# Performance work log

Measured on AMD Instinct MI355X. Metric: run time of the kernel, lower is better.

The kernel has to match this reference:

```python
import jax, jax.numpy as jnp
import numpy as np

B, S, DIM = 1, 1024, 1024
H, G = 16, 4
HPG = H // G
DK = 64
DV = 64
L_CMP, D_STR = 32, 16      # compression block length l, stride d
L_SEL, N_SEL = 64, 8       # selection block length, num selected blocks
W_WIN = 512                # sliding window
TAU = 1.0
GATE_H = 32
SCALE = 1.0 / float(np.sqrt(DK))
S_CMP = (S - L_CMP) // D_STR + 1          # number of compressed blocks
N_BLK = (S + L_SEL - 1) // L_SEL          # number of selection blocks

# static Eq.9 mapping: fractional overlap of compressed block c with selection block m
_c0 = np.arange(S_CMP) * D_STR
_m0 = np.arange(N_BLK) * L_SEL
_ov = np.maximum(0, np.minimum(_c0[:, None] + L_CMP, _m0[None, :] + L_SEL)
                 - np.maximum(_c0[:, None], _m0[None, :]))
M_MAP = jnp.asarray(_ov.astype(np.float32) / float(L_CMP))   # [S_CMP, N_BLK]

_POOL_IDX = np.arange(S_CMP)[:, None] * D_STR + np.arange(L_CMP)[None, :]  # [S_CMP, L_CMP]


def _rope(x, pos):
    # llama-style rotary embedding; pos broadcasts against x's leading dims
    half = x.shape[-1] // 2
    inv = 1.0 / (10000.0 ** (jnp.arange(half, dtype=jnp.float32) / half))
    ang = pos[..., None] * inv
    cos, sin = jnp.cos(ang), jnp.sin(ang)
    x1, x2 = x[..., :half], x[..., half:]
    return jnp.concatenate([x1 * cos - x2 * sin, x1 * sin + x2 * cos], axis=-1)


def _masked_softmax(scores, mask):
    p = jax.nn.softmax(jnp.where(mask, scores, -1e30), axis=-1)
    return jnp.where(mask.any(axis=-1, keepdims=True), p, 0.0)


def _forward(x, wq, wk_sel, wv_sel, wk_win, wv_win, wk_cmp, wv_cmp, w_out,
             g1_w, g1_b, g2_w, g2_b):
    pos = jnp.arange(S, dtype=jnp.float32)
    t = jnp.arange(S)
    q = _rope((x @ wq.T).reshape(B, S, G, HPG, DK), pos[None, :, None, None])  # [B,S,G,h,Dk]

    def k_proj(w):
        k = jnp.transpose((x @ w.T).reshape(B, S, G, DK), (0, 2, 1, 3))  # [B,G,S,Dk]
        return _rope(k, pos[None, None, :])

    def v_proj(w):
        return jnp.transpose((x @ w.T).reshape(B, S, G, DV), (0, 2, 1, 3))  # [B,G,S,Dv]

    # --- compressed branch (phi = avg pooling over blocks of l with stride d) ---
    k_cmp = k_proj(wk_cmp); v_cmp = v_proj(wv_cmp)
    Kc = k_cmp[:, :, _POOL_IDX, :].mean(axis=3)  # [B,G,S_CMP,Dk]
    Vc = v_cmp[:, :, _POOL_IDX, :].mean(axis=3)  # [B,G,S_CMP,Dv]
    sc_cmp = jnp.einsum('bsghd,bgcd->bsghc', q, Kc) * SCALE
    cmp_mask = (jnp.arange(S_CMP) * D_STR + (L_CMP - 1))[None, :] <= t[:, None]  # [S,S_CMP]
    p_cmp = _masked_softmax(sc_cmp, cmp_mask[None, :, None, None, :])
    O_cmp = jnp.einsum('bsghc,bgcd->bsghd', p_cmp, Vc)

    # --- selection branch: map compressed scores to selection blocks (Eq.9),
    #     group-sum over heads, force block 0 + current block, top-k, gather ---
    p_slc = jnp.einsum('bsghc,cm->bsgm', p_cmp, M_MAP)  # sums over heads h -> [B,S,G,N_BLK]
    blk = jnp.arange(N_BLK)
    forced = (blk[None, :] == 0) | (blk[None, :] == (t // L_SEL)[:, None])  # [S,N_BLK]
    causal = (blk[None, :] * L_SEL) <= t[:, None]                            # [S,N_BLK]
    sel_logits = jnp.where(causal[None, :, None, :],
                           p_slc + 1e6 * forced[None, :, None, :], -1e9)
    _, top_idx = jax.lax.top_k(sel_logits, N_SEL)  # [B,S,G,N_SEL]
    tok = (top_idx[..., None] * L_SEL + jnp.arange(L_SEL)).reshape(B, S, G, N_SEL * L_SEL)
    tok_g = jnp.transpose(tok, (0, 2, 1, 3))  # [B,G,S,L]
    k_sel = k_proj(wk_sel); v_sel = v_proj(wv_sel)
    bi = jnp.arange(B)[:, None, None, None]
    gi = jnp.arange(G)[None, :, None, None]
    Kg = k_sel[bi, gi, tok_g]  # [B,G,S,L,Dk]
    Vg = v_sel[bi, gi, tok_g]  # [B,G,S,L,Dv]
    sc_sel = jnp.einsum('bsghd,bgsld->bsghl', q, Kg) * SCALE
    tok_mask = (tok <= t[None, :, None, None])[:, :, :, None, :]  # causal within gathered tokens
    p_sel = _masked_softmax(sc_sel, tok_mask)
    O_sel = jnp.einsum('bsghl,bgsld->bsghd', p_sel, Vg)

    # --- sliding window branch ---
    k_win = k_proj(wk_win); v_win = v_proj(wv_win)
    sc_win = jnp.einsum('bsghd,bgtd->bsght', q, k_win) * SCALE
    wmask = (t[None, :] <= t[:, None]) & (t[None, :] > t[:, None] - W_WIN)  # [S,S]
    p_win = _masked_softmax(sc_win, wmask[None, :, None, None, :])
    O_win = jnp.einsum('bsght,bgtd->bsghd', p_win, v_win)

    # --- gate MLP on group-pooled q ---
    qg = q.mean(axis=3)                              # [B,S,G,Dk]
    h1 = jax.nn.silu(qg @ g1_w.T + g1_b)
    glog = (h1 @ g2_w.T + g2_b) / max(TAU, 1e-6)
    pg = jax.nn.softmax(glog, axis=-1)               # [B,S,G,3]
    top2 = jax.lax.top_k(glog, 2)[0]
    peaked = jax.lax.stop_gradient((top2[..., 0] - top2[..., 1]) > 50.0)
    onehot = jax.nn.one_hot(jnp.argmax(glog, axis=-1), 3, dtype=pg.dtype)
    pg = jnp.where(peaked[..., None], onehot, pg)

    O = (pg[..., 0][..., None, None] * O_cmp
         + pg[..., 1][..., None, None] * O_sel
         + pg[..., 2][..., None, None] * O_win)      # [B,S,G,h,Dv]
    return O.reshape(B, S, H * DV) @ w_out.T


def setup_inputs() -> dict:
    key = jax.random.key(0)
    ks = jax.random.split(key, 11)
    n = lambda k, shp, s=0.02: jax.random.normal(k, shp, dtype=jnp.float32) * s
    return {
        'x': jax.random.normal(ks[0], (B, S, DIM), dtype=jnp.float32),
        'wq': n(ks[1], (H * DK, DIM)),
        'wk_sel': n(ks[2], (G * DK, DIM)),
        'wv_sel': n(ks[3], (G * DV, DIM)),
        'wk_win': n(ks[4], (G * DK, DIM)),
        'wv_win': n(ks[5], (G * DV, DIM)),
        'wk_cmp': n(ks[6], (G * DK, DIM)),
        'wv_cmp': n(ks[7], (G * DV, DIM)),
        'w_out': n(ks[8], (DIM, H * DV)),
        'g1_w': n(ks[9], (GATE_H, DK), 0.1),
        'g1_b': jnp.zeros((GATE_H,), jnp.float32),
        'g2_w': n(ks[10], (3, GATE_H), 0.05),  # xavier gain 0.1 -> small init
        'g2_b': jnp.zeros((3,), jnp.float32),
    }


def reference(x, wq, wk_sel, wv_sel, wk_win, wv_win, wk_cmp, wv_cmp, w_out,
              g1_w, g1_b, g2_w, g2_b):
    return _forward(x, wq, wk_sel, wv_sel, wk_win, wv_win, wk_cmp, wv_cmp, w_out,
                    g1_w, g1_b, g2_w, g2_b)
```

## Files before the change

### kernel.cpp

```cpp
#include <hip/hip_runtime.h>
#include <math.h>

#define SLEN   1024
#define NGRP   4
#define NHEAD  16
#define HPGRP  4
#define DKV    64
#define SCMP   63
#define NBLK   16
#define NSELK  8
#define WWIN   512
#define SCALEF 0.125f
#define QBLK   16
#define EXPOFF 8.0f

typedef __attribute__((ext_vector_type(4))) float f32x4;
typedef __attribute__((ext_vector_type(8))) short bf16x8;

__device__ __forceinline__ unsigned short f2bf(float f) {
  unsigned u = __float_as_uint(f);
  u += 0x7FFFu + ((u >> 16) & 1u);
  return (unsigned short)(u >> 16);
}
__device__ __forceinline__ unsigned pack2(float a, float b) {
  return (unsigned)f2bf(a) | ((unsigned)f2bf(b) << 16);
}
__device__ __forceinline__ bf16x8 pack8(float4 a, float4 b) {
  union { bf16x8 v; unsigned u[4]; } u;
  u.u[0] = pack2(a.x, a.y); u.u[1] = pack2(a.z, a.w);
  u.u[2] = pack2(b.x, b.y); u.u[3] = pack2(b.z, b.w);
  return u.v;
}

struct ConvJobs {
  const float* src[9];
  unsigned* dst[9];
  int n4[9];
  int cnt;
};

__global__ __launch_bounds__(256) void conv_f32_bf16(ConvJobs jb) {
  const int stride = gridDim.x * blockDim.x;
  for (int t = 0; t < jb.cnt; ++t) {
    const float4* s = (const float4*)jb.src[t];
    uint2* d = (uint2*)jb.dst[t];
    const int n4 = jb.n4[t];
    for (int i = blockIdx.x * blockDim.x + threadIdx.x; i < n4; i += stride) {
      const float4 v = s[i];
      uint2 o;
      o.x = pack2(v.x, v.y);
      o.y = pack2(v.z, v.w);
      d[i] = o;
    }
  }
}

__global__ __launch_bounds__(256) void conv_add_bf16(
    const float* __restrict__ a, const float* __restrict__ b, uint2* __restrict__ d)
{
  const int i = blockIdx.x * 256 + threadIdx.x;
  const float4 va = ((const float4*)a)[i];
  const float4 vb = ((const float4*)b)[i];
  uint2 o;
  o.x = pack2(va.x + vb.x, va.y + vb.y);
  o.y = pack2(va.z + vb.z, va.w + vb.w);
  d[i] = o;
}

__device__ __forceinline__ void gload_lds16(const unsigned short* g, unsigned short* l) {
  __builtin_amdgcn_global_load_lds(
      (const __attribute__((address_space(1))) void*)g,
      (__attribute__((address_space(3))) void*)l, 16, 0, 0);
}

__device__ __forceinline__ void gemm_mfma_body(
    const unsigned short* __restrict__ A, const unsigned short* __restrict__ W,
    float* __restrict__ C, int N, int K, int bm, int bn, int tid)
{
  __shared__ unsigned short As[3][2048];
  __shared__ unsigned short Bs[3][2048];
  const int lane = tid & 63;
  const int wave = tid >> 6;
  const int wr = wave >> 1, wc = wave & 1;

  const int sub = tid >> 6;
  const int kh  = (tid >> 4) & 3;
  const int row = tid & 15;
  const unsigned short* aSrc = A + (size_t)(bm + sub * 16 + row) * K + kh * 8;
  const unsigned short* bSrc = W + (size_t)(bn + sub * 16 + row) * K + kh * 8;
  const int slot = tid * 8;

  f32x4 acc[2][2];
#pragma unroll
  for (int m = 0; m < 2; ++m)
#pragma unroll
    for (int n = 0; n < 2; ++n) acc[m][n] = (f32x4){0.f, 0.f, 0.f, 0.f};

  const int NIT = K >> 5;
  gload_lds16(aSrc + 0,  &As[0][slot]);
  gload_lds16(bSrc + 0,  &Bs[0][slot]);
  gload_lds16(aSrc + 32, &As[1][slot]);
  gload_lds16(bSrc + 32, &Bs[1][slot]);

  for (int i = 0; i < NIT; ++i) {
    __builtin_amdgcn_sched_barrier(0);
    if (i + 1 < NIT) asm volatile("s_waitcnt vmcnt(2)" ::: "memory");
    else             asm volatile("s_waitcnt vmcnt(0)" ::: "memory");
    __builtin_amdgcn_s_barrier();
    __builtin_amdgcn_sched_barrier(0);
    if (i + 2 < NIT) {
      const int nb = (i + 2) % 3;
      gload_lds16(aSrc + (i + 2) * 32, &As[nb][slot]);
      gload_lds16(bSrc + (i + 2) * 32, &Bs[nb][slot]);
    }
    const int cur = i % 3;
    const bf16x8 a0 = *(const bf16x8*)(&As[cur][(wr * 2 + 0) * 512 + lane * 8]);
    const bf16x8 a1 = *(const bf16x8*)(&As[cur][(wr * 2 + 1) * 512 + lane * 8]);
    const bf16x8 b0 = *(const bf16x8*)(&Bs[cur][(wc * 2 + 0) * 512 + lane * 8]);
    const bf16x8 b1 = *(const bf16x8*)(&Bs[cur][(wc * 2 + 1) * 512 + lane * 8]);
    acc[0][0] = __builtin_amdgcn_mfma_f32_16x16x32_bf16(a0, b0, acc[0][0], 0, 0, 0);
    acc[0][1] = __builtin_amdgcn_mfma_f32_16x16x32_bf16(a0, b1, acc[0][1], 0, 0, 0);
    acc[1][0] = __builtin_amdgcn_mfma_f32_16x16x32_bf16(a1, b0, acc[1][0], 0, 0, 0);
    acc[1][1] = __builtin_amdgcn_mfma_f32_16x16x32_bf16(a1, b1, acc[1][1], 0, 0, 0);
  }

  const int cr = (lane >> 4) * 4;
  const int cc = lane & 15;
#pragma unroll
  for (int m = 0; m < 2; ++m)
#pragma unroll
    for (int n = 0; n < 2; ++n) {
      float* cp = C + (size_t)(bm + wr * 32 + m * 16 + cr) * N + (bn + wc * 32 + n * 16 + cc);
#pragma unroll
      for (int r = 0; r < 4; ++r) cp[(size_t)r * N] = acc[m][n][r];
    }
}

__global__ __launch_bounds__(256) void gemm_bf16(
    const unsigned short* __restrict__ A, const unsigned short* __restrict__ W,
    float* __restrict__ C, int N, int K)
{
  gemm_mfma_body(A, W, C, N, K, blockIdx.y * 64, blockIdx.x * 64, threadIdx.x);
}

struct W6 { const unsigned short* w[6]; };

__global__ __launch_bounds__(256) void gemm_bf16_kv6(
    const unsigned short* __restrict__ A, W6 p6, float* __restrict__ Cbase)
{
  gemm_mfma_body(A, p6.w[blockIdx.z], Cbase + (size_t)blockIdx.z * (SLEN * 256),
                 256, 1024, blockIdx.y * 64, blockIdx.x * 64, threadIdx.x);
}

__global__ __launch_bounds__(256) void prep_kernel(
    const float* __restrict__ qf,
    const float* __restrict__ kself,
    const float* __restrict__ kwinf,
    const float* __restrict__ g1w, const float* __restrict__ g1b,
    const float* __restrict__ g2w, const float* __restrict__ g2b,
    unsigned short* __restrict__ q_b,
    unsigned short* __restrict__ kselb, unsigned short* __restrict__ kwinb,
    float* __restrict__ gates, float2* __restrict__ tab)
{
  const int s = blockIdx.x, t = threadIdx.x;
  __shared__ float csS[32], snS[32];
  __shared__ float qs[1024];
  __shared__ float qgS[4][64];
  __shared__ float h1S[4][32];
  __shared__ float glS[4][3];
  if (t < 32) {
    const float inv = powf(10000.f, -(float)t * (1.f / 32.f));
    float sn, cs;
    sincosf((float)s * inv, &sn, &cs);
    csS[t] = cs; snS[t] = sn;
    tab[s * 32 + t] = make_float2(cs, sn);
  }
  __syncthreads();
  {
    const int ht = t >> 4;
    const float* qr = qf + (size_t)s * 1024 + ht * 64;
#pragma unroll
    for (int i = 0; i < 2; ++i) {
      const int dd = (t & 15) * 2 + i;
      const float x1 = qr[dd], x2 = qr[dd + 32];
      qs[ht * 64 + dd]      = x1 * csS[dd] - x2 * snS[dd];
      qs[ht * 64 + dd + 32] = x1 * snS[dd] + x2 * csS[dd];
    }
  }
  {
    const int which = t >> 7;
    const int g = (t >> 5) & 3, dd = t & 31;
    const float* src = (which ? kwinf : kself) + (size_t)s * 256 + g * 64;
    unsigned short* dst = (which ? kwinb : kselb) + (size_t)s * 256 + g * 64;
    const float x1 = src[dd], x2 = src[dd + 32];
    dst[dd]      = f2bf(x1 * csS[dd] - x2 * snS[dd]);
    dst[dd + 32] = f2bf(x1 * snS[dd] + x2 * csS[dd]);
  }
  __syncthreads();
  {
    uint2 o;
    o.x = pack2(qs[t * 4 + 0], qs[t * 4 + 1]);
    o.y = pack2(qs[t * 4 + 2], qs[t * 4 + 3]);
    *(uint2*)(q_b + (size_t)s * 1024 + t * 4) = o;
  }
  {
    const int g = t >> 6, d = t & 63;
    qgS[g][d] = (qs[g * 256 + d] + qs[g * 256 + 64 + d] +
                 qs[g * 256 + 128 + d] + qs[g * 256 + 192 + d]) * 0.25f;
  }
  __syncthreads();
  if (t < 128) {
    const int g = t >> 5, j = t & 31;
    float a = g1b[j];
    for (int d = 0; d < 64; ++d) a += qgS[g][d] * g1w[j * 64 + d];
    h1S[g][j] = a / (1.f + expf(-a));
  }
  __syncthreads();
  if (t < 16) {
    const int g = t >> 2, rr = t & 3;
    if (rr < 3) {
      float a = g2b[rr];
      for (int j = 0; j < 32; ++j) a += h1S[g][j] * g2w[rr * 32 + j];
      glS[g][rr] = a;
    }
  }
  __syncthreads();
  if (t < 4) {
    const int g = t;
    const float gl0 = glS[g][0], gl1 = glS[g][1], gl2 = glS[g][2];
    const float m1 = fmaxf(gl0, fmaxf(gl1, gl2));
    const float e0 = expf(gl0 - m1), e1 = expf(gl1 - m1), e2 = expf(gl2 - m1);
    const float inv = 1.f / (e0 + e1 + e2);
    float p0 = e0 * inv, p1 = e1 * inv, p2 = e2 * inv;
    int am = 0; float best = gl0;
    if (gl1 > best) { best = gl1; am = 1; }
    if (gl2 > best) { best = gl2; am = 2; }
    float second = -INFINITY;
    if (am != 0) second = fmaxf(second, gl0);
    if (am != 1) second = fmaxf(second, gl1);
    if (am != 2) second = fmaxf(second, gl2);
    if (best - second > 50.f) {
      p0 = (am == 0) ? 1.f : 0.f; p1 = (am == 1) ? 1.f : 0.f; p2 = (am == 2) ? 1.f : 0.f;
    }
    float* o = gates + (size_t)(s * 4 + g) * 3;
    o[0] = p0; o[1] = p1; o[2] = p2;
  }
}

__global__ __launch_bounds__(64) void pool_kernel(
    const float* __restrict__ kcmp, const float* __restrict__ vcmp,
    const float2* __restrict__ tab,
    unsigned short* __restrict__ KcB, unsigned short* __restrict__ VcTB)
{
  const int c = blockIdx.x;
  const int g = blockIdx.y;
  const int d = threadIdx.x;
  float ak = 0.f, av = 0.f;
  if (c < SCMP) {
    const int d2 = d & 31;
    for (int j = 0; j < 32; ++j) {
      const int pos = c * 16 + j;
      const float2 t2 = tab[pos * 32 + d2];
      const float k1 = kcmp[(size_t)pos * 256 + g * 64 + d2];
      const float k2 = kcmp[(size_t)pos * 256 + g * 64 + d2 + 32];
      ak += (d < 32) ? (k1 * t2.x - k2 * t2.y) : (k1 * t2.y + k2 * t2.x);
      av += vcmp[(size_t)pos * 256 + g * 64 + d];
    }
    ak *= (1.f / 32.f); av *= (1.f / 32.f);
  }
  KcB[(size_t)(g * 64 + c) * 64 + d] = f2bf(ak);
  VcTB[(size_t)(g * 64 + d) * 64 + c] = f2bf(av);
}

__global__ __launch_bounds__(256) void transpose_v(
    const float* __restrict__ v0, const float* __restrict__ v1,
    unsigned short* __restrict__ t0, unsigned short* __restrict__ t1)
{
  const float* src = blockIdx.z ? v1 : v0;
  unsigned short* dst = blockIdx.z ? t1 : t0;
  __shared__ float tile[32][33];
  const int tr = blockIdx.x * 32, tc = blockIdx.y * 32;
  const int r = threadIdx.x >> 5, c = threadIdx.x & 31;
#pragma unroll
  for (int i = 0; i < 4; ++i)
    tile[r + i * 8][c] = src[(size_t)(tr + r + i * 8) * 256 + tc + c];
  __syncthreads();
#pragma unroll
  for (int i = 0; i < 4; ++i)
    dst[(size_t)(tc + r + i * 8) * 1024 + tr + c] = f2bf(tile[c][r + i * 8]);
}

__device__ __forceinline__ void stage_tile(
    const unsigned short* kbase, int krow,
    const unsigned short* vbase, int vrow,
    unsigned short* Kb, unsigned short* Vb, int tid)
{
#pragma unroll
  for (int i = 0; i < 2; ++i) {
    const int t2 = tid + i * 256;
    const int sf = t2 >> 7, sks = (t2 >> 6) & 1, skh = (t2 >> 4) & 3, stk = t2 & 15;
    gload_lds16(kbase + (size_t)(16 * sf + stk) * krow + sks * 32 + skh * 8, Kb + t2 * 8);
    gload_lds16(vbase + (size_t)(16 * sf + stk) * vrow + sks * 32 + skh * 8, Vb + t2 * 8);
  }
}

template<int BR>
__device__ __forceinline__ void attn_compute(
    int b, int s0, int l,
    bf16x8 aq0, bf16x8 aq1,
    float (&ps)[4], f32x4 (&Oa)[4],
    const unsigned short* Klds, const unsigned short* Vlds,
    float (*Pw)[68], const unsigned* selmaskS)
{
  const int kg = l >> 4, lr = l & 15;
  f32x4 sc[4];
  __builtin_amdgcn_s_setprio(1);
#pragma unroll
  for (int f = 0; f < 4; ++f) {
    sc[f] = (f32x4){0.f, 0.f, 0.f, 0.f};
    sc[f] = __builtin_amdgcn_mfma_f32_16x16x32_bf16(
        aq0, *(const bf16x8*)(Klds + (f * 2 + 0) * 512 + l * 8), sc[f], 0, 0, 0);
    sc[f] = __builtin_amdgcn_mfma_f32_16x16x32_bf16(
        aq1, *(const bf16x8*)(Klds + (f * 2 + 1) * 512 + l * 8), sc[f], 0, 0, 0);
  }
  __builtin_amdgcn_s_setprio(0);

#pragma unroll
  for (int r = 0; r < 4; ++r) {
    const int lrow = kg * 4 + r;
    const int sr = s0 + lrow;
#pragma unroll
    for (int f = 0; f < 4; ++f) {
      const int tok = b * 64 + 16 * f + lr;
      bool ok;
      if (BR == 0)      ok = (tok < SCMP) && (tok * 16 + 31 <= sr);
      else if (BR == 1) ok = ((selmaskS[lrow] >> b) & 1u) && (tok <= sr);
      else              ok = (tok <= sr) && (tok > sr - WWIN);
      const float p = ok ? __expf(sc[f][r] * SCALEF - EXPOFF) : 0.f;
      Pw[lrow][16 * f + lr] = p;
      ps[r] += p;
    }
  }
  asm volatile("s_waitcnt lgkmcnt(0)" ::: "memory");
#pragma unroll
  for (int ks = 0; ks < 2; ++ks) {
    const float4 pa0 = *(const float4*)&Pw[lr][ks * 32 + kg * 8];
    const float4 pa1 = *(const float4*)&Pw[lr][ks * 32 + kg * 8 + 4];
    const bf16x8 pa = pack8(pa0, pa1);
    __builtin_amdgcn_s_setprio(1);
#pragma unroll
    for (int f = 0; f < 4; ++f)
      Oa[f] = __builtin_amdgcn_mfma_f32_16x16x32_bf16(
          pa, *(const bf16x8*)(Vlds + (f * 2 + ks) * 512 + l * 8), Oa[f], 0, 0, 0);
    __builtin_amdgcn_s_setprio(0);
  }
}

__global__ __launch_bounds__(256) void attn_mfma_kernel(
    const unsigned short* __restrict__ qb,
    const unsigned short* __restrict__ kselb,
    const unsigned short* __restrict__ vselT,
    const unsigned short* __restrict__ kwinb,
    const unsigned short* __restrict__ vwinT,
    const unsigned short* __restrict__ KcB,
    const unsigned short* __restrict__ VcTB,
    const float* __restrict__ gates,
    float* __restrict__ Ocs, float* __restrict__ Owin)
{
  const int qt = blockIdx.x;
  const int g  = blockIdx.y;
  const int z  = blockIdx.z;
  const int s0 = qt * QBLK;
  const int tid = threadIdx.x;
  const int w = tid >> 6, l = tid & 63;
  const int kg = l >> 4, lr = l & 15;
  const int bmax = s0 >> 6;

  __shared__ unsigned short Klds[2][4096];
  __shared__ unsigned short Vlds[2][4096];
  __shared__ float Plds[4][16][68];
  __shared__ float lgS[QBLK][16];
  __shared__ float lcS[4][16];
  __shared__ unsigned selmaskS[QBLK];
  __shared__ int selListS[16];
  __shared__ int nselS;

  if (tid < QBLK) selmaskS[tid] = 0u;

  const int sq = s0 + lr;
  const unsigned short* qrow = qb + (size_t)(sq * 16 + g * 4 + w) * 64;
  const bf16x8 aq0 = *(const bf16x8*)(qrow + kg * 8);
  const bf16x8 aq1 = *(const bf16x8*)(qrow + 32 + kg * 8);

  float gv[3][4];
#pragma unroll
  for (int r = 0; r < 4; ++r) {
    const int sr = s0 + kg * 4 + r;
    const float* gp = gates + (size_t)(sr * 4 + g) * 3;
    gv[0][r] = gp[0]; gv[1][r] = gp[1]; gv[2][r] = gp[2];
  }

  f32x4 Ot[4];
#pragma unroll
  for (int f = 0; f < 4; ++f) Ot[f] = (f32x4){0.f, 0.f, 0.f, 0.f};

  float ps[4], ls[4];
  f32x4 Oa[4];

#define ARESET() do { \
    _Pragma("unroll") for (int r = 0; r < 4; ++r) ps[r] = 0.f; \
    _Pragma("unroll") for (int f = 0; f < 4; ++f) Oa[f] = (f32x4){0.f,0.f,0.f,0.f}; \
  } while (0)
#define REDUCE_LS() do { \
    _Pragma("unroll") for (int r = 0; r < 4; ++r) { \
      ls[r] = ps[r]; \
      ls[r] += __shfl_xor(ls[r], 1); ls[r] += __shfl_xor(ls[r], 2); \
      ls[r] += __shfl_xor(ls[r], 4); ls[r] += __shfl_xor(ls[r], 8); } \
  } while (0)
#define AFINAL(bi) do { \
    _Pragma("unroll") for (int f = 0; f < 4; ++f) \
    _Pragma("unroll") for (int r = 0; r < 4; ++r) \
      Ot[f][r] += gv[bi][r] * ((ls[r] > 0.f) ? (Oa[f][r] / ls[r]) : 0.f); \
  } while (0)

  if (z == 0) {
    ARESET();
    stage_tile(KcB + (size_t)g * 64 * 64, 64, VcTB + (size_t)g * 64 * 64, 64,
               Klds[0], Vlds[0], tid);
    __syncthreads();
    attn_compute<0>(0, s0, l, aq0, aq1, ps, Oa, Klds[0], Vlds[0], Plds[w], selmaskS);
    REDUCE_LS();
    if ((l & 15) == 0) {
#pragma unroll
      for (int r = 0; r < 4; ++r) lcS[w][kg * 4 + r] = ls[r];
    }
    AFINAL(0);
    __syncthreads();

    {
      const int row = tid >> 4, mm = tid & 15;
      float psl = 0.f;
#pragma unroll
      for (int hh = 0; hh < 4; ++hh) {
        const float lc = lcS[hh][row];
        if (lc > 0.f) {
          const int cb = 4 * mm;
          float a = Plds[hh][row][cb] + Plds[hh][row][cb + 1] + Plds[hh][row][cb + 2];
          if (cb >= 1)       a += 0.5f * Plds[hh][row][cb - 1];
          if (cb + 3 < SCMP) a += 0.5f * Plds[hh][row][cb + 3];
          psl += a / lc;
        }
      }
      const bool causal = (mm <= bmax);
      const bool forced = (mm == 0) || (mm == bmax);
      lgS[row][mm] = causal ? (psl + (forced ? 1e6f : 0.f)) : -1e9f;
    }
    __syncthreads();
    {
      const int row = tid >> 4, mm = tid & 15;
      const float my = lgS[row][mm];
      int rank = 0;
#pragma unroll
      for (int m2 = 0; m2 < 16; ++m2) {
        const float v = lgS[row][m2];
        if (v > my || (v == my && m2 < mm)) ++rank;
      }
      if (rank < NSELK && mm <= bmax) atomicOr(&selmaskS[row], 1u << mm);
    }
    __syncthreads();
    if (tid == 0) {
      unsigned u = 0;
      for (int r = 0; r < QBLK; ++r) u |= selmaskS[r];
      int n = 0;
      for (int b = 0; b < 16; ++b) if ((u >> b) & 1u) selListS[n++] = b;
      nselS = n;
    }
    __syncthreads();
    const int nt = nselS;

    ARESET();
    {
      const int b0 = selListS[0];
      stage_tile(kselb + (size_t)b0 * 64 * 256 + g * 64, 256,
                 vselT + (size_t)g * 64 * 1024 + b0 * 64, 1024,
                 Klds[0], Vlds[0], tid);
      __syncthreads();
      for (int i = 0; i < nt; ++i) {
        if (i + 1 < nt) {
          const int bn = selListS[i + 1];
          stage_tile(kselb + (size_t)bn * 64 * 256 + g * 64, 256,
                     vselT + (size_t)g * 64 * 1024 + bn * 64, 1024,
                     Klds[(i + 1) & 1], Vlds[(i + 1) & 1], tid);
        }
        attn_compute<1>(selListS[i], s0, l, aq0, aq1, ps, Oa,
                        Klds[i & 1], Vlds[i & 1], Plds[w], selmaskS);
        __syncthreads();
      }
    }
    REDUCE_LS();
    AFINAL(1);

#pragma unroll
    for (int f = 0; f < 4; ++f)
#pragma unroll
      for (int r = 0; r < 4; ++r) {
        const int sr = s0 + kg * 4 + r;
        Ocs[(size_t)(sr * 16 + g * 4 + w) * 64 + 16 * f + lr] = Ot[f][r];
      }
  } else {
    ARESET();
    const int blo = (s0 >= (WWIN - 1)) ? ((s0 - (WWIN - 1)) >> 6) : 0;
    const int nt = bmax - blo + 1;
    stage_tile(kwinb + (size_t)blo * 64 * 256 + g * 64, 256,
               vwinT + (size_t)g * 64 * 1024 + blo * 64, 1024,
               Klds[0], Vlds[0], tid);
    __syncthreads();
    for (int i = 0; i < nt; ++i) {
      if (i + 1 < nt) {
        const int bn = blo + i + 1;
        stage_tile(kwinb + (size_t)bn * 64 * 256 + g * 64, 256,
                   vwinT + (size_t)g * 64 * 1024 + bn * 64, 1024,
                   Klds[(i + 1) & 1], Vlds[(i + 1) & 1], tid);
      }
      attn_compute<2>(blo + i, s0, l, aq0, aq1, ps, Oa,
                      Klds[i & 1], Vlds[i & 1], Plds[w], selmaskS);
      __syncthreads();
    }
    REDUCE_LS();
    AFINAL(2);

#pragma unroll
    for (int f = 0; f < 4; ++f)
#pragma unroll
      for (int r = 0; r < 4; ++r) {
        const int sr = s0 + kg * 4 + r;
        Owin[(size_t)(sr * 16 + g * 4 + w) * 64 + 16 * f + lr] = Ot[f][r];
      }
  }
#undef ARESET
#undef REDUCE_LS
#undef AFINAL
}

extern "C" void kernel_launch(void* const* d_in, const int* in_sizes, int n_in,
                              void* d_out, int out_size, void* d_ws, size_t ws_size,
                              hipStream_t stream) {
  const float* x      = (const float*)d_in[0];
  const float* wq     = (const float*)d_in[1];
  const float* wk_sel = (const float*)d_in[2];
  const float* wv_sel = (const float*)d_in[3];
  const float* wk_win = (const float*)d_in[4];
  const float* wv_win = (const float*)d_in[5];
  const float* wk_cmp = (const float*)d_in[6];
  const float* wv_cmp = (const float*)d_in[7];
  const float* w_out  = (const float*)d_in[8];
  const float* g1w    = (const float*)d_in[9];
  const float* g1b    = (const float*)d_in[10];
  const float* g2w    = (const float*)d_in[11];
  const float* g2b    = (const float*)d_in[12];

  float* ws = (float*)d_ws;
  float* q     = ws;
  float* kv    = q + 1048576;
  float* ksel  = kv;
  float* vsel  = kv + 1 * 262144;
  float* kwin  = kv + 2 * 262144;
  float* vwin  = kv + 3 * 262144;
  float* kcmp  = kv + 4 * 262144;
  float* vcmp  = kv + 5 * 262144;
  float* gts   = kv + 6 * 262144;
  float* Obuf  = gts + 12288;
  float* Owin  = kv;
  float2* tab  = (float2*)Obuf;

  unsigned short* xb     = (unsigned short*)(Obuf + 1048576);
  unsigned short* wqb    = xb + 1048576;
  unsigned short* kvwb   = wqb + 1048576;
  unsigned short* w_outb = kvwb + 6 * 262144;
  unsigned short* q_b    = w_outb + 1048576;
  unsigned short* kselb  = q_b + 1048576;
  unsigned short* kwinb  = kselb + 262144;
  unsigned short* vselT  = kwinb + 262144;
  unsigned short* vwinT  = vselT + 262144;
  unsigned short* KcB    = vwinT + 262144;
  unsigned short* VcTB   = KcB + 16384;

  ConvJobs j1 = {};
  j1.cnt = 9;
  j1.src[0] = x;      j1.dst[0] = (unsigned*)xb;                j1.n4[0] = 262144;
  j1.src[1] = wq;     j1.dst[1] = (unsigned*)wqb;               j1.n4[1] = 262144;
  j1.src[2] = wk_sel; j1.dst[2] = (unsigned*)(kvwb + 0*262144); j1.n4[2] = 65536;
  j1.src[3] = wv_sel; j1.dst[3] = (unsigned*)(kvwb + 1*262144); j1.n4[3] = 65536;
  j1.src[4] = wk_win; j1.dst[4] = (unsigned*)(kvwb + 2*262144); j1.n4[4] = 65536;
  j1.src[5] = wv_win; j1.dst[5] = (unsigned*)(kvwb + 3*262144); j1.n4[5] = 65536;
  j1.src[6] = wk_cmp; j1.dst[6] = (unsigned*)(kvwb + 4*262144); j1.n4[6] = 65536;
  j1.src[7] = wv_cmp; j1.dst[7] = (unsigned*)(kvwb + 5*262144); j1.n4[7] = 65536;
  j1.src[8] = w_out;  j1.dst[8] = (unsigned*)w_outb;            j1.n4[8] = 262144;
  conv_f32_bf16<<<1024, 256, 0, stream>>>(j1);

  gemm_bf16<<<dim3(16, 16), 256, 0, stream>>>(xb, wqb, q, 1024, 1024);
  W6 p6 = {{ kvwb + 0*262144, kvwb + 1*262144, kvwb + 2*262144,
             kvwb + 3*262144, kvwb + 4*262144, kvwb + 5*262144 }};
  gemm_bf16_kv6<<<dim3(4, 16, 6), 256, 0, stream>>>(xb, p6, kv);

  prep_kernel<<<1024, 256, 0, stream>>>(q, ksel, kwin, g1w, g1b, g2w, g2b,
                                        q_b, kselb, kwinb, gts, tab);

  pool_kernel<<<dim3(64, 4), 64, 0, stream>>>(kcmp, vcmp, tab, KcB, VcTB);

  transpose_v<<<dim3(32, 8, 2), 256, 0, stream>>>(vsel, vwin, vselT, vwinT);

  attn_mfma_kernel<<<dim3(64, 4, 2), 256, 0, stream>>>(
      q_b, kselb, vselT, kwinb, vwinT, KcB, VcTB, gts, Obuf, Owin);

  conv_add_bf16<<<1024, 256, 0, stream>>>(Obuf, Owin, (uint2*)xb);
  gemm_bf16<<<dim3(16, 16), 256, 0, stream>>>(xb, w_outb, (float*)d_out, 1024, 1024);
}
```

Measured before the change: 122.4 us.

## Fuse Q/KV projections into one GEMM, merge prep kernels, triple-buffer attention tiles

```diff
diff --git a/kernel.cpp b/kernel.cpp
--- a/kernel.cpp
+++ b/kernel.cpp
@@ -13,6 +13,7 @@
 #define SCALEF 0.125f
 #define QBLK   16
 #define EXPOFF 8.0f
+#define CSTR   2560
 
 typedef __attribute__((ext_vector_type(4))) float f32x4;
 typedef __attribute__((ext_vector_type(8))) short bf16x8;
@@ -143,151 +144,148 @@
   gemm_mfma_body(A, W, C, N, K, blockIdx.y * 64, blockIdx.x * 64, threadIdx.x);
 }
 
-struct W6 { const unsigned short* w[6]; };
-
-__global__ __launch_bounds__(256) void gemm_bf16_kv6(
-    const unsigned short* __restrict__ A, W6 p6, float* __restrict__ Cbase)
-{
-  gemm_mfma_body(A, p6.w[blockIdx.z], Cbase + (size_t)blockIdx.z * (SLEN * 256),
-                 256, 1024, blockIdx.y * 64, blockIdx.x * 64, threadIdx.x);
-}
-
-__global__ __launch_bounds__(256) void prep_kernel(
-    const float* __restrict__ qf,
-    const float* __restrict__ kself,
-    const float* __restrict__ kwinf,
+__global__ __launch_bounds__(256) void mid_kernel(
+    const float* __restrict__ C,
     const float* __restrict__ g1w, const float* __restrict__ g1b,
     const float* __restrict__ g2w, const float* __restrict__ g2b,
     unsigned short* __restrict__ q_b,
     unsigned short* __restrict__ kselb, unsigned short* __restrict__ kwinb,
-    float* __restrict__ gates, float2* __restrict__ tab)
+    float* __restrict__ gates,
+    unsigned short* __restrict__ vselT, unsigned short* __restrict__ vwinT,
+    unsigned short* __restrict__ KcB, unsigned short* __restrict__ VcTB)
 {
-  const int s = blockIdx.x, t = threadIdx.x;
+  const int b = blockIdx.x;
+  const int t = threadIdx.x;
+
   __shared__ float csS[32], snS[32];
   __shared__ float qs[1024];
   __shared__ float qgS[4][64];
   __shared__ float h1S[4][32];
   __shared__ float glS[4][3];
-  if (t < 32) {
-    const float inv = powf(10000.f, -(float)t * (1.f / 32.f));
-    float sn, cs;
-    sincosf((float)s * inv, &sn, &cs);
-    csS[t] = cs; snS[t] = sn;
-    tab[s * 32 + t] = make_float2(cs, sn);
-  }
-  __syncthreads();
-  {
-    const int ht = t >> 4;
-    const float* qr = qf + (size_t)s * 1024 + ht * 64;
-#pragma unroll
-    for (int i = 0; i < 2; ++i) {
-      const int dd = (t & 15) * 2 + i;
-      const float x1 = qr[dd], x2 = qr[dd + 32];
-      qs[ht * 64 + dd]      = x1 * csS[dd] - x2 * snS[dd];
-      qs[ht * 64 + dd + 32] = x1 * snS[dd] + x2 * csS[dd];
-    }
-  }
-  {
-    const int which = t >> 7;
-    const int g = (t >> 5) & 3, dd = t & 31;
-    const float* src = (which ? kwinf : kself) + (size_t)s * 256 + g * 64;
-    unsigned short* dst = (which ? kwinb : kselb) + (size_t)s * 256 + g * 64;
-    const float x1 = src[dd], x2 = src[dd + 32];
-    dst[dd]      = f2bf(x1 * csS[dd] - x2 * snS[dd]);
-    dst[dd + 32] = f2bf(x1 * snS[dd] + x2 * csS[dd]);
-  }
-  __syncthreads();
-  {
-    uint2 o;
-    o.x = pack2(qs[t * 4 + 0], qs[t * 4 + 1]);
-    o.y = pack2(qs[t * 4 + 2], qs[t * 4 + 3]);
-    *(uint2*)(q_b + (size_t)s * 1024 + t * 4) = o;
-  }
-  {
+  __shared__ float tile[32][33];
+  __shared__ float csP[32][32], snP[32][32];
+
+  if (b < 1024) {
+    const int s = b;
+    if (t < 32) {
+      const float inv = powf(10000.f, -(float)t * (1.f / 32.f));
+      float sn, cs;
+      sincosf((float)s * inv, &sn, &cs);
+      csS[t] = cs; snS[t] = sn;
+    }
+    __syncthreads();
+    {
+      const int ht = t >> 4;
+      const float* qr = C + (size_t)s * CSTR + ht * 64;
+#pragma unroll
+      for (int i = 0; i < 2; ++i) {
+        const int dd = (t & 15) * 2 + i;
+        const float x1 = qr[dd], x2 = qr[dd + 32];
+        qs[ht * 64 + dd]      = x1 * csS[dd] - x2 * snS[dd];
+        qs[ht * 64 + dd + 32] = x1 * snS[dd] + x2 * csS[dd];
+      }
+    }
+    {
+      const int which = t >> 7;
+      const int g = (t >> 5) & 3, dd = t & 31;
+      const float* src = C + (size_t)s * CSTR + (which ? 1536 : 1024) + g * 64;
+      unsigned short* dst = (which ? kwinb : kselb) + (size_t)s * 256 + g * 64;
+      const float x1 = src[dd], x2 = src[dd + 32];
+      dst[dd]      = f2bf(x1 * csS[dd] - x2 * snS[dd]);
+      dst[dd + 32] = f2bf(x1 * snS[dd] + x2 * csS[dd]);
+    }
+    __syncthreads();
+    {
+      uint2 o;
+      o.x = pack2(qs[t * 4 + 0], qs[t * 4 + 1]);
+      o.y = pack2(qs[t * 4 + 2], qs[t * 4 + 3]);
+      *(uint2*)(q_b + (size_t)s * 1024 + t * 4) = o;
+    }
+    {
+      const int g = t >> 6, d = t & 63;
+      qgS[g][d] = (qs[g * 256 + d] + qs[g * 256 + 64 + d] +
+                   qs[g * 256 + 128 + d] + qs[g * 256 + 192 + d]) * 0.25f;
+    }
+    __syncthreads();
+    if (t < 128) {
+      const int g = t >> 5, j = t & 31;
+      float a = g1b[j];
+      for (int d = 0; d < 64; ++d) a += qgS[g][d] * g1w[j * 64 + d];
+      h1S[g][j] = a / (1.f + expf(-a));
+    }
+    __syncthreads();
+    if (t < 16) {
+      const int g = t >> 2, rr = t & 3;
+      if (rr < 3) {
+        float a = g2b[rr];
+        for (int j = 0; j < 32; ++j) a += h1S[g][j] * g2w[rr * 32 + j];
+        glS[g][rr] = a;
+      }
+    }
+    __syncthreads();
+    if (t < 4) {
+      const int g = t;
+      const float gl0 = glS[g][0], gl1 = glS[g][1], gl2 = glS[g][2];
+      const float m1 = fmaxf(gl0, fmaxf(gl1, gl2));
+      const float e0 = expf(gl0 - m1), e1 = expf(gl1 - m1), e2 = expf(gl2 - m1);
+      const float inv = 1.f / (e0 + e1 + e2);
+      float p0 = e0 * inv, p1 = e1 * inv, p2 = e2 * inv;
+      int am = 0; float best = gl0;
+      if (gl1 > best) { best = gl1; am = 1; }
+      if (gl2 > best) { best = gl2; am = 2; }
+      float second = -INFINITY;
+      if (am != 0) second = fmaxf(second, gl0);
+      if (am != 1) second = fmaxf(second, gl1);
+      if (am != 2) second = fmaxf(second, gl2);
+      if (best - second > 50.f) {
+        p0 = (am == 0) ? 1.f : 0.f; p1 = (am == 1) ? 1.f : 0.f; p2 = (am == 2) ? 1.f : 0.f;
+      }
+      float* o = gates + (size_t)(s * 4 + g) * 3;
+      o[0] = p0; o[1] = p1; o[2] = p2;
+    }
+  } else if (b < 1536) {
+    const int idx = b - 1024;
+    const int tr = (idx & 31) * 32, tc = ((idx >> 5) & 7) * 32;
+    const int z = idx >> 8;
+    const int off = z ? 1792 : 1280;
+    unsigned short* dst = z ? vwinT : vselT;
+    const int r = t >> 5, c = t & 31;
+#pragma unroll
+    for (int i = 0; i < 4; ++i)
+      tile[r + i * 8][c] = C[(size_t)(tr + r + i * 8) * CSTR + off + tc + c];
+    __syncthreads();
+#pragma unroll
+    for (int i = 0; i < 4; ++i)
+      dst[(size_t)(tc + r + i * 8) * 1024 + tr + c] = f2bf(tile[c][r + i * 8]);
+  } else {
+    const int c = b - 1536;
     const int g = t >> 6, d = t & 63;
-    qgS[g][d] = (qs[g * 256 + d] + qs[g * 256 + 64 + d] +
-                 qs[g * 256 + 128 + d] + qs[g * 256 + 192 + d]) * 0.25f;
-  }
-  __syncthreads();
-  if (t < 128) {
-    const int g = t >> 5, j = t & 31;
-    float a = g1b[j];
-    for (int d = 0; d < 64; ++d) a += qgS[g][d] * g1w[j * 64 + d];
-    h1S[g][j] = a / (1.f + expf(-a));
-  }
-  __syncthreads();
-  if (t < 16) {
-    const int g = t >> 2, rr = t & 3;
-    if (rr < 3) {
-      float a = g2b[rr];
-      for (int j = 0; j < 32; ++j) a += h1S[g][j] * g2w[rr * 32 + j];
-      glS[g][rr] = a;
-    }
-  }
-  __syncthreads();
-  if (t < 4) {
-    const int g = t;
-    const float gl0 = glS[g][0], gl1 = glS[g][1], gl2 = glS[g][2];
-    const float m1 = fmaxf(gl0, fmaxf(gl1, gl2));
-    const float e0 = expf(gl0 - m1), e1 = expf(gl1 - m1), e2 = expf(gl2 - m1);
-    const float inv = 1.f / (e0 + e1 + e2);
-    float p0 = e0 * inv, p1 = e1 * inv, p2 = e2 * inv;
-    int am = 0; float best = gl0;
-    if (gl1 > best) { best = gl1; am = 1; }
-    if (gl2 > best) { best = gl2; am = 2; }
-    float second = -INFINITY;
-    if (am != 0) second = fmaxf(second, gl0);
-    if (am != 1) second = fmaxf(second, gl1);
-    if (am != 2) second = fmaxf(second, gl2);
-    if (best - second > 50.f) {
-      p0 = (am == 0) ? 1.f : 0.f; p1 = (am == 1) ? 1.f : 0.f; p2 = (am == 2) ? 1.f : 0.f;
-    }
-    float* o = gates + (size_t)(s * 4 + g) * 3;
-    o[0] = p0; o[1] = p1; o[2] = p2;
-  }
-}
-
-__global__ __launch_bounds__(64) void pool_kernel(
-    const float* __restrict__ kcmp, const float* __restrict__ vcmp,
-    const float2* __restrict__ tab,
-    unsigned short* __restrict__ KcB, unsigned short* __restrict__ VcTB)
-{
-  const int c = blockIdx.x;
-  const int g = blockIdx.y;
-  const int d = threadIdx.x;
-  float ak = 0.f, av = 0.f;
-  if (c < SCMP) {
-    const int d2 = d & 31;
-    for (int j = 0; j < 32; ++j) {
-      const int pos = c * 16 + j;
-      const float2 t2 = tab[pos * 32 + d2];
-      const float k1 = kcmp[(size_t)pos * 256 + g * 64 + d2];
-      const float k2 = kcmp[(size_t)pos * 256 + g * 64 + d2 + 32];
-      ak += (d < 32) ? (k1 * t2.x - k2 * t2.y) : (k1 * t2.y + k2 * t2.x);
-      av += vcmp[(size_t)pos * 256 + g * 64 + d];
-    }
-    ak *= (1.f / 32.f); av *= (1.f / 32.f);
-  }
-  KcB[(size_t)(g * 64 + c) * 64 + d] = f2bf(ak);
-  VcTB[(size_t)(g * 64 + d) * 64 + c] = f2bf(av);
-}
-
-__global__ __launch_bounds__(256) void transpose_v(
-    const float* __restrict__ v0, const float* __restrict__ v1,
-    unsigned short* __restrict__ t0, unsigned short* __restrict__ t1)
-{
-  const float* src = blockIdx.z ? v1 : v0;
-  unsigned short* dst = blockIdx.z ? t1 : t0;
-  __shared__ float tile[32][33];
-  const int tr = blockIdx.x * 32, tc = blockIdx.y * 32;
-  const int r = threadIdx.x >> 5, c = threadIdx.x & 31;
-#pragma unroll
-  for (int i = 0; i < 4; ++i)
-    tile[r + i * 8][c] = src[(size_t)(tr + r + i * 8) * 256 + tc + c];
-  __syncthreads();
-#pragma unroll
-  for (int i = 0; i < 4; ++i)
-    dst[(size_t)(tc + r + i * 8) * 1024 + tr + c] = f2bf(tile[c][r + i * 8]);
+#pragma unroll
+    for (int qq = 0; qq < 4; ++qq) {
+      const int idx = t * 4 + qq;
+      const int j = idx >> 5, dd = idx & 31;
+      const float inv = powf(10000.f, -(float)dd * (1.f / 32.f));
+      float sn, cs;
+      sincosf((float)(c * 16 + j) * inv, &sn, &cs);
+      csP[j][dd] = cs; snP[j][dd] = sn;
+    }
+    __syncthreads();
+    float ak = 0.f, av = 0.f;
+    if (c < SCMP) {
+      const int d2 = d & 31;
+      for (int j = 0; j < 32; ++j) {
+        const int pos = c * 16 + j;
+        const float k1 = C[(size_t)pos * CSTR + 2048 + g * 64 + d2];
+        const float k2 = C[(size_t)pos * CSTR + 2048 + g * 64 + d2 + 32];
+        ak += (d < 32) ? (k1 * csP[j][d2] - k2 * snP[j][d2])
+                       : (k1 * snP[j][d2] + k2 * csP[j][d2]);
+        av += C[(size_t)pos * CSTR + 2304 + g * 64 + d];
+      }
+      ak *= (1.f / 32.f); av *= (1.f / 32.f);
+    }
+    KcB[(size_t)(g * 64 + c) * 64 + d] = f2bf(ak);
+    VcTB[(size_t)(g * 64 + d) * 64 + c] = f2bf(av);
+  }
 }
 
 __device__ __forceinline__ void stage_tile(
@@ -355,6 +353,15 @@
     __builtin_amdgcn_s_setprio(0);
   }
 }
+
+#define TILE_SYNC(more) do { \
+    __builtin_amdgcn_sched_barrier(0); \
+    if (more) asm volatile("s_waitcnt vmcnt(4)" ::: "memory"); \
+    else      asm volatile("s_waitcnt vmcnt(0)" ::: "memory"); \
+    __builtin_amdgcn_sched_barrier(0); \
+    __builtin_amdgcn_s_barrier(); \
+    __builtin_amdgcn_sched_barrier(0); \
+  } while (0)
 
 __global__ __launch_bounds__(256) void attn_mfma_kernel(
     const unsigned short* __restrict__ qb,
@@ -376,8 +383,8 @@
   const int kg = l >> 4, lr = l & 15;
   const int bmax = s0 >> 6;
 
-  __shared__ unsigned short Klds[2][4096];
-  __shared__ unsigned short Vlds[2][4096];
+  __shared__ unsigned short Klds[3][4096];
+  __shared__ unsigned short Vlds[3][4096];
   __shared__ float Plds[4][16][68];
   __shared__ float lgS[QBLK][16];
   __shared__ float lcS[4][16];
@@ -427,7 +434,7 @@
     ARESET();
     stage_tile(KcB + (size_t)g * 64 * 64, 64, VcTB + (size_t)g * 64 * 64, 64,
                Klds[0], Vlds[0], tid);
-    __syncthreads();
+    TILE_SYNC(0);
     attn_compute<0>(0, s0, l, aq0, aq1, ps, Oa, Klds[0], Vlds[0], Plds[w], selmaskS);
     REDUCE_LS();
     if ((l & 15) == 0) {
@@ -484,17 +491,18 @@
       stage_tile(kselb + (size_t)b0 * 64 * 256 + g * 64, 256,
                  vselT + (size_t)g * 64 * 1024 + b0 * 64, 1024,
                  Klds[0], Vlds[0], tid);
-      __syncthreads();
       for (int i = 0; i < nt; ++i) {
         if (i + 1 < nt) {
           const int bn = selListS[i + 1];
+          const int nb = (i + 1) % 3;
           stage_tile(kselb + (size_t)bn * 64 * 256 + g * 64, 256,
                      vselT + (size_t)g * 64 * 1024 + bn * 64, 1024,
-                     Klds[(i + 1) & 1], Vlds[(i + 1) & 1], tid);
+                     Klds[nb], Vlds[nb], tid);
         }
+        TILE_SYNC(i + 1 < nt);
         attn_compute<1>(selListS[i], s0, l, aq0, aq1, ps, Oa,
-                        Klds[i & 1], Vlds[i & 1], Plds[w], selmaskS);
-        __syncthreads();
+                        Klds[i % 3], Vlds[i % 3], Plds[w], selmaskS);
+        __builtin_amdgcn_sched_barrier(0);
       }
     }
     REDUCE_LS();
@@ -514,17 +522,18 @@
     stage_tile(kwinb + (size_t)blo * 64 * 256 + g * 64, 256,
                vwinT + (size_t)g * 64 * 1024 + blo * 64, 1024,
                Klds[0], Vlds[0], tid);
-    __syncthreads();
     for (int i = 0; i < nt; ++i) {
       if (i + 1 < nt) {
         const int bn = blo + i + 1;
+        const int nb = (i + 1) % 3;
         stage_tile(kwinb + (size_t)bn * 64 * 256 + g * 64, 256,
                    vwinT + (size_t)g * 64 * 1024 + bn * 64, 1024,
-                   Klds[(i + 1) & 1], Vlds[(i + 1) & 1], tid);
-      }
+                   Klds[nb], Vlds[nb], tid);
+      }
+      TILE_SYNC(i + 1 < nt);
       attn_compute<2>(blo + i, s0, l, aq0, aq1, ps, Oa,
-                      Klds[i & 1], Vlds[i & 1], Plds[w], selmaskS);
-      __syncthreads();
+                      Klds[i % 3], Vlds[i % 3], Plds[w], selmaskS);
+      __builtin_amdgcn_sched_barrier(0);
     }
     REDUCE_LS();
     AFINAL(2);
@@ -560,23 +569,14 @@
   const float* g2b    = (const float*)d_in[12];
 
   float* ws = (float*)d_ws;
-  float* q     = ws;
-  float* kv    = q + 1048576;
-  float* ksel  = kv;
-  float* vsel  = kv + 1 * 262144;
-  float* kwin  = kv + 2 * 262144;
-  float* vwin  = kv + 3 * 262144;
-  float* kcmp  = kv + 4 * 262144;
-  float* vcmp  = kv + 5 * 262144;
-  float* gts   = kv + 6 * 262144;
-  float* Obuf  = gts + 12288;
-  float* Owin  = kv;
-  float2* tab  = (float2*)Obuf;
-
-  unsigned short* xb     = (unsigned short*)(Obuf + 1048576);
-  unsigned short* wqb    = xb + 1048576;
-  unsigned short* kvwb   = wqb + 1048576;
-  unsigned short* w_outb = kvwb + 6 * 262144;
+  float* Cq    = ws;
+  float* gts   = Cq + 2621440;
+  float* Ocs   = gts + 12288;
+  float* Owin  = Ocs + 1048576;
+
+  unsigned short* xb     = (unsigned short*)(Owin + 1048576);
+  unsigned short* wqkvb  = xb + 1048576;
+  unsigned short* w_outb = wqkvb + 2621440;
   unsigned short* q_b    = w_outb + 1048576;
   unsigned short* kselb  = q_b + 1048576;
   unsigned short* kwinb  = kselb + 262144;
@@ -587,32 +587,26 @@
 
   ConvJobs j1 = {};
   j1.cnt = 9;
-  j1.src[0] = x;      j1.dst[0] = (unsigned*)xb;                j1.n4[0] = 262144;
-  j1.src[1] = wq;     j1.dst[1] = (unsigned*)wqb;               j1.n4[1] = 262144;
-  j1.src[2] = wk_sel; j1.dst[2] = (unsigned*)(kvwb + 0*262144); j1.n4[2] = 65536;
-  j1.src[3] = wv_sel; j1.dst[3] = (unsigned*)(kvwb + 1*262144); j1.n4[3] = 65536;
-  j1.src[4] = wk_win; j1.dst[4] = (unsigned*)(kvwb + 2*262144); j1.n4[4] = 65536;
-  j1.src[5] = wv_win; j1.dst[5] = (unsigned*)(kvwb + 3*262144); j1.n4[5] = 65536;
-  j1.src[6] = wk_cmp; j1.dst[6] = (unsigned*)(kvwb + 4*262144); j1.n4[6] = 65536;
-  j1.src[7] = wv_cmp; j1.dst[7] = (unsigned*)(kvwb + 5*262144); j1.n4[7] = 65536;
-  j1.src[8] = w_out;  j1.dst[8] = (unsigned*)w_outb;            j1.n4[8] = 262144;
+  j1.src[0] = x;      j1.dst[0] = (unsigned*)xb;                        j1.n4[0] = 262144;
+  j1.src[1] = wq;     j1.dst[1] = (unsigned*)wqkvb;                     j1.n4[1] = 262144;
+  j1.src[2] = wk_sel; j1.dst[2] = (unsigned*)(wqkvb + 1048576);         j1.n4[2] = 65536;
+  j1.src[3] = wv_sel; j1.dst[3] = (unsigned*)(wqkvb + 1048576+262144);  j1.n4[3] = 65536;
+  j1.src[4] = wk_win; j1.dst[4] = (unsigned*)(wqkvb + 1048576+524288);  j1.n4[4] = 65536;
+  j1.src[5] = wv_win; j1.dst[5] = (unsigned*)(wqkvb + 1048576+786432);  j1.n4[5] = 65536;
+  j1.src[6] = wk_cmp; j1.dst[6] = (unsigned*)(wqkvb + 1048576+1048576); j1.n4[6] = 65536;
+  j1.src[7] = wv_cmp; j1.dst[7] = (unsigned*)(wqkvb + 1048576+1310720); j1.n4[7] = 65536;
+  j1.src[8] = w_out;  j1.dst[8] = (unsigned*)w_outb;                    j1.n4[8] = 262144;
   conv_f32_bf16<<<1024, 256, 0, stream>>>(j1);
 
-  gemm_bf16<<<dim3(16, 16), 256, 0, stream>>>(xb, wqb, q, 1024, 1024);
-  W6 p6 = {{ kvwb + 0*262144, kvwb + 1*262144, kvwb + 2*262144,
-             kvwb + 3*262144, kvwb + 4*262144, kvwb + 5*262144 }};
-  gemm_bf16_kv6<<<dim3(4, 16, 6), 256, 0, stream>>>(xb, p6, kv);
-
-  prep_kernel<<<1024, 256, 0, stream>>>(q, ksel, kwin, g1w, g1b, g2w, g2b,
-                                        q_b, kselb, kwinb, gts, tab);
-
-  pool_kernel<<<dim3(64, 4), 64, 0, stream>>>(kcmp, vcmp, tab, KcB, VcTB);
-
-  transpose_v<<<dim3(32, 8, 2), 256, 0, stream>>>(vsel, vwin, vselT, vwinT);
+  gemm_bf16<<<dim3(40, 16), 256, 0, stream>>>(xb, wqkvb, Cq, CSTR, 1024);
+
+  mid_kernel<<<1600, 256, 0, stream>>>(Cq, g1w, g1b, g2w, g2b,
+                                       q_b, kselb, kwinb, gts,
+                                       vselT, vwinT, KcB, VcTB);
 
   attn_mfma_kernel<<<dim3(64, 4, 2), 256, 0, stream>>>(
-      q_b, kselb, vselT, kwinb, vwinT, KcB, VcTB, gts, Obuf, Owin);
-
-  conv_add_bf16<<<1024, 256, 0, stream>>>(Obuf, Owin, (uint2*)xb);
+      q_b, kselb, vselT, kwinb, vwinT, KcB, VcTB, gts, Ocs, Owin);
+
+  conv_add_bf16<<<1024, 256, 0, stream>>>(Ocs, Owin, (uint2*)xb);
   gemm_bf16<<<dim3(16, 16), 256, 0, stream>>>(xb, w_outb, (float*)d_out, 1024, 1024);
 }
```

Result: faster. 112.7 us (-7.9%).
